# Kernel optimization log

Hardware: AMD Instinct MI355X
Metric: run time of the kernel (lower is better)

The kernel has to match this reference:

```python
import jax, jax.numpy as jnp
from jax import lax
import numpy as np

J = 10       # transition_window
S = 1000     # posterior_samples
T = 50000    # forecast_days


def setup_inputs() -> dict:
    key = jax.random.key(0)
    k1, k2, k3, k4, k5 = jax.random.split(key, 5)
    # r_t near 1 so the multiplicative recurrence stays in a sane range
    r_t = 1.0 + 0.02 * (jax.random.uniform(k1, (1, T), dtype=jnp.float32) - 0.5)
    # warmup asymptomatic counts (positive, constrained via softplus in original)
    warmup_A = 1.0 + 100.0 * jax.random.uniform(k2, (J, S), dtype=jnp.float32)
    # serial interval, positive, ~5 days
    T_serial = 3.0 + 4.0 * jax.random.uniform(k3, (S,), dtype=jnp.float32)
    # rho_M in (0,1) (sigmoid-constrained in original)
    rho_M = jax.random.uniform(k4, (S,), dtype=jnp.float32)
    # pi_M: per-sample transition-delay pmf over J days (normalized over axis 0)
    pi_raw = jax.random.uniform(k5, (J, S), dtype=jnp.float32) + 0.1
    pi_M = pi_raw / jnp.sum(pi_raw, axis=0, keepdims=True)
    return {"r_t": r_t, "warmup_A": warmup_A, "T_serial": T_serial,
            "rho_M": rho_M, "pi_M": pi_M}


def reference(r_t, warmup_A, T_serial, rho_M, pi_M):
    """Faithful vectorized forward of CovidModel.call for Vax.total.

    A[d] = A[d-1] * r_t[d]^(1/T_serial),  A[-1..-J] = warmup_A
    M[d] = rho_M * sum_j pi_M[j] * A[d-j-1]
    Returns M stacked: (T, S).
    """
    r = jnp.squeeze(r_t)                                   # (T,)
    # per-day multiplicative step, per posterior sample: r_t[d]^(1/T_serial)
    step = jnp.exp(jnp.log(r)[:, None] / T_serial[None, :])  # (T, S)

    def day_step(carry, s):
        a = carry * s
        return a, a

    _, A = lax.scan(day_step, warmup_A[-1], step)          # (T, S)

    # extended flux history: warmup days then forecast days
    A_ext = jnp.concatenate([warmup_A, A], axis=0)         # (J+T, S)

    # windowed weighted sum (causal conv over the delay window):
    # M[d] = rho_M * sum_j pi_M[j] * A_ext[J + d - j - 1]
    M = jnp.zeros_like(A)
    for j in range(J):  # J is a small fixed window
        M = M + pi_M[j][None, :] * lax.dynamic_slice_in_dim(A_ext, J - 1 - j, A.shape[0], axis=0)
    M = M * rho_M[None, :]
    return M
```

## Files before the change

kernel.cpp:

```cpp
#include <hip/hip_runtime.h>
#include <hip/hip_bf16.h>
#include <math.h>


#define SCAN_BS 1024

typedef float v4f __attribute__((ext_vector_type(4)));

__global__ void scan_blocks_kernel(const float* __restrict__ r, int T,
                                   double* __restrict__ Lpart,
                                   double* __restrict__ blockSums) {
    __shared__ double sh[SCAN_BS];
    const int i = blockIdx.x * SCAN_BS + threadIdx.x;
    double v = (i < T) ? (double)log2f(r[i]) : 0.0;
    sh[threadIdx.x] = v;
    __syncthreads();
    for (int off = 1; off < SCAN_BS; off <<= 1) {
        double u = (threadIdx.x >= off) ? sh[threadIdx.x - off] : 0.0;
        __syncthreads();
        sh[threadIdx.x] += u;
        __syncthreads();
    }
    if (i < T) Lpart[i] = sh[threadIdx.x];
    if (threadIdx.x == SCAN_BS - 1) blockSums[blockIdx.x] = sh[SCAN_BS - 1];
}

__global__ void scan_sums_kernel(const double* __restrict__ blockSums, int nb,
                                 double* __restrict__ offsets) {
    const int lane = threadIdx.x;
    double v = (lane < nb) ? blockSums[lane] : 0.0;
    for (int off = 1; off < 64; off <<= 1) {
        double u = __shfl_up(v, (unsigned)off, 64);
        if (lane >= off) v += u;
    }
    double excl = __shfl_up(v, 1u, 64);
    if (lane == 0) excl = 0.0;
    if (lane < nb) offsets[lane] = excl;
}

__global__ void scan_apply_kernel(const double* __restrict__ Lpart,
                                  const double* __restrict__ offsets,
                                  float* __restrict__ L, int T) {
    const int i = blockIdx.x * SCAN_BS + threadIdx.x;
    if (i < T) L[i] = (float)(Lpart[i] + offsets[blockIdx.x]);
}

template <int J, bool CHECK>
__global__ __launch_bounds__(256)
void forecast4_kernel(const float* __restrict__ L,
                      const float* __restrict__ warmup_A,
                      const float* __restrict__ T_serial,
                      const float* __restrict__ rho_M,
                      const float* __restrict__ pi_M,
                      float* __restrict__ out,
                      int d0_base, int T, int S, int dchunk) {
    const int q = blockIdx.x * blockDim.x + threadIdx.x;
    const int s = q * 4;
    if (s + 3 >= S) return;

    const int d0   = d0_base + blockIdx.y * dchunk;
    const int dend = CHECK ? min(d0 + dchunk, T) : (d0 + dchunk);

    const float4 ts  = *reinterpret_cast<const float4*>(&T_serial[s]);
    const float4 rho = *reinterpret_cast<const float4*>(&rho_M[s]);
    const float4 wA4 = *reinterpret_cast<const float4*>(&warmup_A[(J - 1) * S + s]);

    float invT[4] = {1.f / ts.x, 1.f / ts.y, 1.f / ts.z, 1.f / ts.w};
    float wA[4]   = {wA4.x, wA4.y, wA4.z, wA4.w};
    float scl[4]  = {rho.x * wA[0], rho.y * wA[1], rho.z * wA[2], rho.w * wA[3]};
    float invW[4] = {1.f / wA[0], 1.f / wA[1], 1.f / wA[2], 1.f / wA[3]};

    float pis[J][4];
#pragma unroll
    for (int j = 0; j < J; ++j) {
        const float4 p = *reinterpret_cast<const float4*>(&pi_M[j * S + s]);
        pis[j][0] = p.x * scl[0]; pis[j][1] = p.y * scl[1];
        pis[j][2] = p.z * scl[2]; pis[j][3] = p.w * scl[3];
    }

    float a[J][4];
#pragma unroll
    for (int i = 0; i < J; ++i) {
        const int t = d0 - J + i;
        if (t >= 0) {
            const float Lt = L[t];
#pragma unroll
            for (int c = 0; c < 4; ++c) a[i][c] = exp2f(Lt * invT[c]);
        } else {
            const float4 w = *reinterpret_cast<const float4*>(&warmup_A[(J + t) * S + s]);
            a[i][0] = w.x * invW[0]; a[i][1] = w.y * invW[1];
            a[i][2] = w.z * invW[2]; a[i][3] = w.w * invW[3];
        }
    }

    for (int db = d0; db < dend; db += J) {
#pragma unroll
        for (int k = 0; k < J; ++k) {
            const int d = db + k;
            if (!CHECK || d < dend) {
                float m[4] = {0.f, 0.f, 0.f, 0.f};
#pragma unroll
                for (int j = 0; j < J; ++j) {
                    const int slot = (J + k - 1 - j) % J;
#pragma unroll
                    for (int c = 0; c < 4; ++c) m[c] = fmaf(pis[j][c], a[slot][c], m[c]);
                }
                v4f mv;
                mv.x = m[0]; mv.y = m[1]; mv.z = m[2]; mv.w = m[3];
                *reinterpret_cast<v4f*>(&out[(size_t)d * S + s]) = mv;
                const float Ld = L[d];
#pragma unroll
                for (int c = 0; c < 4; ++c) a[k][c] = exp2f(Ld * invT[c]);
            }
        }
    }
}

template <int J>
__global__ __launch_bounds__(64)
void forecast_scalar_kernel(const float* __restrict__ L,
                            const float* __restrict__ warmup_A,
                            const float* __restrict__ T_serial,
                            const float* __restrict__ rho_M,
                            const float* __restrict__ pi_M,
                            float* __restrict__ out,
                            int T, int S, int s0, int dchunk) {
    const int s = s0 + blockIdx.x * blockDim.x + threadIdx.x;
    if (s >= S) return;
    const int d0   = blockIdx.y * dchunk;
    const int dend = min(d0 + dchunk, T);

    const float invT = 1.0f / T_serial[s];
    const float wA   = warmup_A[(J - 1) * S + s];
    const float scl  = rho_M[s] * wA;
    const float invW = 1.0f / wA;

    float pis[J];
#pragma unroll
    for (int j = 0; j < J; ++j) pis[j] = pi_M[j * S + s] * scl;

    float a[J];
#pragma unroll
    for (int i = 0; i < J; ++i) {
        const int t = d0 - J + i;
        a[i] = (t >= 0) ? exp2f(L[t] * invT)
                        : warmup_A[(J + t) * S + s] * invW;
    }
    for (int db = d0; db < dend; db += J) {
#pragma unroll
        for (int k = 0; k < J; ++k) {
            const int d = db + k;
            if (d < dend) {
                float m = 0.0f;
#pragma unroll
                for (int j = 0; j < J; ++j) m = fmaf(pis[j], a[(J + k - 1 - j) % J], m);
                out[(size_t)d * S + s] = m;
                a[k] = exp2f(L[d] * invT);
            }
        }
    }
}

extern "C" void kernel_launch(void* const* d_in, const int* in_sizes, int n_in,
                              void* d_out, int out_size, void* d_ws, size_t ws_size,
                              hipStream_t stream) {
    const float* r_t      = (const float*)d_in[0];
    const float* warmup_A = (const float*)d_in[1];
    const float* T_serial = (const float*)d_in[2];
    const float* rho_M    = (const float*)d_in[3];
    const float* pi_M     = (const float*)d_in[4];
    float* out            = (float*)d_out;

    const int T = in_sizes[0];
    const int S = in_sizes[2];
    const int nb = (T + SCAN_BS - 1) / SCAN_BS;

    char* ws = (char*)d_ws;
    double* Lpart   = (double*)ws;
    double* bsums   = (double*)(ws + ((size_t)T * 8 + 255) / 256 * 256);
    double* offsets = bsums + 64;
    float*  L       = (float*)(offsets + 64);

    scan_blocks_kernel<<<nb, SCAN_BS, 0, stream>>>(r_t, T, Lpart, bsums);
    scan_sums_kernel<<<1, 64, 0, stream>>>(bsums, nb, offsets);
    scan_apply_kernel<<<nb, SCAN_BS, 0, stream>>>(Lpart, offsets, L, T);

    const int dchunk = 50;
    const int quads = S / 4;
    const int fullChunks = T / dchunk;
    const int dTailStart = fullChunks * dchunk;

    if (quads > 0) {
        dim3 block(256, 1, 1);
        if (fullChunks > 0) {
            dim3 grid((quads + 255) / 256, fullChunks, 1);
            forecast4_kernel<10, false><<<grid, block, 0, stream>>>(
                L, warmup_A, T_serial, rho_M, pi_M, out, 0, T, S, dchunk);
        }
        if (dTailStart < T) {
            dim3 grid((quads + 255) / 256, 1, 1);
            forecast4_kernel<10, true><<<grid, block, 0, stream>>>(
                L, warmup_A, T_serial, rho_M, pi_M, out, dTailStart, T, S, dchunk);
        }
    }
    const int tail = S - quads * 4;
    if (tail > 0) {
        dim3 block(64, 1, 1);
        dim3 grid(1, (T + dchunk - 1) / dchunk, 1);
        forecast_scalar_kernel<10><<<grid, block, 0, stream>>>(L, warmup_A, T_serial,
                                                               rho_M, pi_M, out, T, S,
                                                               quads * 4, dchunk);
    }
}
```

Baseline: 215.2 us.

## Use wave-shuffle block scan, fold block-sum scan into apply, batch L loads

```diff
diff --git a/kernel.cpp b/kernel.cpp
--- a/kernel.cpp
+++ b/kernel.cpp
@@ -7,42 +7,58 @@
 
 typedef float v4f __attribute__((ext_vector_type(4)));
 
-__global__ void scan_blocks_kernel(const float* __restrict__ r, int T,
-                                   double* __restrict__ Lpart,
-                                   double* __restrict__ blockSums) {
-    __shared__ double sh[SCAN_BS];
-    const int i = blockIdx.x * SCAN_BS + threadIdx.x;
+__global__ __launch_bounds__(SCAN_BS)
+void scan_blocks_kernel(const float* __restrict__ r, int T,
+                        double* __restrict__ Lpart,
+                        double* __restrict__ blockSums) {
+    __shared__ double waveSums[16];
+    const int i    = blockIdx.x * SCAN_BS + threadIdx.x;
+    const int lane = threadIdx.x & 63;
+    const int wid  = threadIdx.x >> 6;
+
     double v = (i < T) ? (double)log2f(r[i]) : 0.0;
-    sh[threadIdx.x] = v;
-    __syncthreads();
-    for (int off = 1; off < SCAN_BS; off <<= 1) {
-        double u = (threadIdx.x >= off) ? sh[threadIdx.x - off] : 0.0;
-        __syncthreads();
-        sh[threadIdx.x] += u;
-        __syncthreads();
-    }
-    if (i < T) Lpart[i] = sh[threadIdx.x];
-    if (threadIdx.x == SCAN_BS - 1) blockSums[blockIdx.x] = sh[SCAN_BS - 1];
-}
-
-__global__ void scan_sums_kernel(const double* __restrict__ blockSums, int nb,
-                                 double* __restrict__ offsets) {
-    const int lane = threadIdx.x;
-    double v = (lane < nb) ? blockSums[lane] : 0.0;
+#pragma unroll
     for (int off = 1; off < 64; off <<= 1) {
         double u = __shfl_up(v, (unsigned)off, 64);
         if (lane >= off) v += u;
     }
-    double excl = __shfl_up(v, 1u, 64);
-    if (lane == 0) excl = 0.0;
-    if (lane < nb) offsets[lane] = excl;
-}
-
-__global__ void scan_apply_kernel(const double* __restrict__ Lpart,
-                                  const double* __restrict__ offsets,
-                                  float* __restrict__ L, int T) {
+    if (lane == 63) waveSums[wid] = v;
+    __syncthreads();
+    if (wid == 0) {
+        double w = (lane < 16) ? waveSums[lane] : 0.0;
+#pragma unroll
+        for (int off = 1; off < 16; off <<= 1) {
+            double u = __shfl_up(w, (unsigned)off, 64);
+            if (lane >= off) w += u;
+        }
+        if (lane < 16) waveSums[lane] = w;
+    }
+    __syncthreads();
+    if (wid > 0) v += waveSums[wid - 1];
+    if (i < T) Lpart[i] = v;
+    if (threadIdx.x == SCAN_BS - 1) blockSums[blockIdx.x] = v;
+}
+
+__global__ __launch_bounds__(SCAN_BS)
+void scan_apply_kernel(const double* __restrict__ Lpart,
+                       const double* __restrict__ blockSums, int nb,
+                       float* __restrict__ L, int T) {
+    __shared__ double offSh;
+    if (threadIdx.x < 64) {
+        double v = ((int)threadIdx.x < nb) ? blockSums[threadIdx.x] : 0.0;
+#pragma unroll
+        for (int off = 1; off < 64; off <<= 1) {
+            double u = __shfl_up(v, (unsigned)off, 64);
+            if ((int)threadIdx.x >= off) v += u;
+        }
+        double excl = 0.0;
+        if (blockIdx.x > 0) excl = __shfl(v, (int)blockIdx.x - 1, 64);
+        if (threadIdx.x == 0) offSh = excl;
+    }
+    __syncthreads();
+    const double off = offSh;
     const int i = blockIdx.x * SCAN_BS + threadIdx.x;
-    if (i < T) L[i] = (float)(Lpart[i] + offsets[blockIdx.x]);
+    if (i < T) L[i] = (float)(Lpart[i] + off);
 }
 
 template <int J, bool CHECK>
@@ -94,6 +110,14 @@
     }
 
     for (int db = d0; db < dend; db += J) {
+        float Lg[J];
+        if (!CHECK) {
+#pragma unroll
+            for (int k = 0; k < J; ++k) Lg[k] = L[db + k];
+        } else {
+#pragma unroll
+            for (int k = 0; k < J; ++k) Lg[k] = (db + k < T) ? L[db + k] : 0.0f;
+        }
 #pragma unroll
         for (int k = 0; k < J; ++k) {
             const int d = db + k;
@@ -108,9 +132,8 @@
                 v4f mv;
                 mv.x = m[0]; mv.y = m[1]; mv.z = m[2]; mv.w = m[3];
                 *reinterpret_cast<v4f*>(&out[(size_t)d * S + s]) = mv;
-                const float Ld = L[d];
-#pragma unroll
-                for (int c = 0; c < 4; ++c) a[k][c] = exp2f(Ld * invT[c]);
+#pragma unroll
+                for (int c = 0; c < 4; ++c) a[k][c] = exp2f(Lg[k] * invT[c]);
             }
         }
     }
@@ -176,16 +199,14 @@
     const int nb = (T + SCAN_BS - 1) / SCAN_BS;
 
     char* ws = (char*)d_ws;
-    double* Lpart   = (double*)ws;
-    double* bsums   = (double*)(ws + ((size_t)T * 8 + 255) / 256 * 256);
-    double* offsets = bsums + 64;
-    float*  L       = (float*)(offsets + 64);
+    double* Lpart = (double*)ws;
+    double* bsums = (double*)(ws + ((size_t)T * 8 + 255) / 256 * 256);
+    float*  L     = (float*)(bsums + 64);
 
     scan_blocks_kernel<<<nb, SCAN_BS, 0, stream>>>(r_t, T, Lpart, bsums);
-    scan_sums_kernel<<<1, 64, 0, stream>>>(bsums, nb, offsets);
-    scan_apply_kernel<<<nb, SCAN_BS, 0, stream>>>(Lpart, offsets, L, T);
-
-    const int dchunk = 50;
+    scan_apply_kernel<<<nb, SCAN_BS, 0, stream>>>(Lpart, bsums, nb, L, T);
+
+    const int dchunk = 40;
     const int quads = S / 4;
     const int fullChunks = T / dchunk;
     const int dTailStart = fullChunks * dchunk;
```

New measurement: 210.8 us. 2.1% less time.
